# Optimization experiments

Measured on AMD Instinct MI355X. Metric: run time of the kernel, lower is better.

## Reference

```python
import jax, jax.numpy as jnp
import numpy as np

N_HEADS = 32
N_KV_HEADS = 8


def _rope_tables(T, half_dim):
    # standard rotary angle tables: theta_i = 10000^(-2i/D)
    inv_freq = 1.0 / (10000.0 ** (np.arange(half_dim, dtype=np.float32) / half_dim))
    ang = np.arange(T, dtype=np.float32)[:, None] * inv_freq[None, :]  # [T, D/2]
    return jnp.asarray(np.sin(ang)), jnp.asarray(np.cos(ang))


def setup_inputs() -> dict:
    key = jax.random.key(0)
    ks = jax.random.split(key, 5)
    B, T, C = 1, 2048, 2048
    hd = C // N_HEADS  # 64
    kv_dim = N_KV_HEADS * hd  # 512
    w_scale = 0.02
    x = jax.random.normal(ks[0], (B, T, C), dtype=jnp.float32)
    Wq = jax.random.normal(ks[1], (C, C), dtype=jnp.float32) * w_scale
    Wk = jax.random.normal(ks[2], (C, kv_dim), dtype=jnp.float32) * w_scale
    Wv = jax.random.normal(ks[3], (C, kv_dim), dtype=jnp.float32) * w_scale
    Wo = jax.random.normal(ks[4], (C, C), dtype=jnp.float32) * w_scale
    rope_sin, rope_cos = _rope_tables(T, hd // 2)
    return {"x": x, "Wq": Wq, "Wk": Wk, "Wv": Wv, "Wo": Wo,
            "rope_sin": rope_sin, "rope_cos": rope_cos, "swa_window": 1024}


def apply_rope(x, sin, cos):
    # x: [B, T, H, D]; sin/cos: [T, D/2]; interleaved-pair rotation
    B, T, H, D = x.shape
    xr = x.reshape(B, T, H, D // 2, 2)
    x1, x2 = xr[..., 0], xr[..., 1]
    s = sin[None, :, None, :]
    c = cos[None, :, None, :]
    o1 = x1 * c - x2 * s
    o2 = x1 * s + x2 * c
    return jnp.stack((o1, o2), axis=-1).reshape(B, T, H, D)


def reference(x, Wq, Wk, Wv, Wo, rope_sin, rope_cos, swa_window):
    B, T, C = x.shape
    hd = C // N_HEADS
    g = N_HEADS // N_KV_HEADS
    q = (x @ Wq).reshape(B, T, N_HEADS, hd)
    k = (x @ Wk).reshape(B, T, N_KV_HEADS, hd)
    v = (x @ Wv).reshape(B, T, N_KV_HEADS, hd)
    q = apply_rope(q, rope_sin, rope_cos)
    k = apply_rope(k, rope_sin, rope_cos)
    # GQA: expand kv heads (repeat_interleave along head dim)
    k = jnp.repeat(k, g, axis=2)
    v = jnp.repeat(v, g, axis=2)
    q = q.transpose(0, 2, 1, 3)  # [B, H, T, D]
    k = k.transpose(0, 2, 1, 3)
    v = v.transpose(0, 2, 1, 3)
    scores = jnp.einsum('bhqd,bhkd->bhqk', q, k) / jnp.sqrt(jnp.float32(hd))
    idx = jnp.arange(T)
    rel = idx[:, None] - idx[None, :]  # query_pos - key_pos
    # masked-out: future tokens (rel < 0) or older than the sliding window
    masked = (rel < 0) | (rel > swa_window)
    scores = jnp.where(masked[None, None], jnp.float32(-1e30), scores)
    attn = jax.nn.softmax(scores, axis=-1)
    out = jnp.einsum('bhqk,bhkd->bhqd', attn, v)
    out = out.transpose(0, 2, 1, 3).reshape(B, T, C)
    return out @ Wo
```

## Files before the change

kernel.cpp:

```cpp
#include <hip/hip_runtime.h>

typedef __attribute__((ext_vector_type(8))) short short8;
typedef __attribute__((ext_vector_type(4))) float f32x4;
typedef unsigned short u16;

#define T_SEQ 2048
#define C_DIM 2048
#define QKV_N 3072
#define HD 64


static __device__ __forceinline__ u16 f2bf(float f) {
    unsigned u = __builtin_bit_cast(unsigned, f);
    unsigned rounding = 0x7fffu + ((u >> 16) & 1u);
    return (u16)((u + rounding) >> 16);
}

static __device__ __forceinline__ void gld_lds16(void* lds, const void* g) {
    __builtin_amdgcn_global_load_lds(
        (const __attribute__((address_space(1))) unsigned int*)g,
        (__attribute__((address_space(3))) unsigned int*)lds, 16, 0, 0);
}


__global__ __launch_bounds__(256) void convert_bf16_k(const float* __restrict__ in,
                                                      u16* __restrict__ out) {
    int i = (blockIdx.x * 256 + threadIdx.x) * 4;
    f32x4 v = *(const f32x4*)(in + i);
    u16* o = out + i;
    o[0] = f2bf(v[0]); o[1] = f2bf(v[1]); o[2] = f2bf(v[2]); o[3] = f2bf(v[3]);
}


__global__ __launch_bounds__(256) void transpose_all(const float* __restrict__ Wq,
                                                     const float* __restrict__ Wk,
                                                     const float* __restrict__ Wv,
                                                     const float* __restrict__ Wo,
                                                     u16* __restrict__ Wt,
                                                     u16* __restrict__ Wot) {
    __shared__ float tile[32][33];
    int bx = blockIdx.x;
    const float* W; u16* D; int N, row_off;
    if (bx < 64)      { W = Wq; D = Wt;  N = 2048; row_off = 0;    }
    else if (bx < 80) { W = Wk; D = Wt;  N = 512;  row_off = 2048; bx -= 64; }
    else if (bx < 96) { W = Wv; D = Wt;  N = 512;  row_off = 2560; bx -= 80; }
    else              { W = Wo; D = Wot; N = 2048; row_off = 0;    bx -= 96; }
    int n0 = bx * 32, k0 = blockIdx.y * 32;
    int tx = threadIdx.x & 31, ty = threadIdx.x >> 5;
#pragma unroll
    for (int i = 0; i < 4; i++)
        tile[ty + i * 8][tx] = W[(size_t)(k0 + ty + i * 8) * N + n0 + tx];
    __syncthreads();
#pragma unroll
    for (int i = 0; i < 4; i++)
        D[(size_t)(row_off + n0 + ty + i * 8) * 2048 + k0 + tx] = f2bf(tile[tx][ty + i * 8]);
}


template <int NF>
__global__ __launch_bounds__(256) void gemm_bt(const u16* __restrict__ A,
                                               const u16* __restrict__ BT,
                                               float* __restrict__ C,
                                               int M, int N, int K) {
    __shared__ alignas(16) u16 As[2][128][64];
    __shared__ alignas(16) u16 Bs[2][32 * NF][64];
    const int m0 = blockIdx.x * 128;
    const int bn0 = blockIdx.y * (32 * NF);
    const int w = threadIdx.x >> 6, lane = threadIdx.x & 63;
    const int lo = lane & 15, hi = lane >> 4;
    const int wr = w >> 1, wc = w & 1;
    const int srcsw = ((lane & 7) ^ (lane >> 3)) * 8;

    f32x4 zero4 = {0.f, 0.f, 0.f, 0.f};
    f32x4 acc[4][NF];
#pragma unroll
    for (int m = 0; m < 4; m++)
#pragma unroll
        for (int n = 0; n < NF; n++) acc[m][n] = zero4;

    const int NSEG = 16 + 4 * NF;
    auto stage = [&](int buf, int k0) {
#pragma unroll
        for (int j = 0; j < NSEG / 4; j++) {
            int s = j * 4 + w;
            if (s < 16) {
                int row = s * 8 + (lane >> 3);
                gld_lds16((char*)&As[buf][0][0] + s * 1024,
                          A + (size_t)(m0 + row) * K + k0 + srcsw);
            } else {
                int s2 = s - 16;
                int row = s2 * 8 + (lane >> 3);
                gld_lds16((char*)&Bs[buf][0][0] + s2 * 1024,
                          BT + (size_t)(bn0 + row) * K + k0 + srcsw);
            }
        }
    };

    stage(0, 0);
    __syncthreads();
    const int nk = K >> 6;
    for (int t = 0; t < nk; t++) {
        const int cur = t & 1;
        if (t + 1 < nk) stage(cur ^ 1, (t + 1) * 64);
#pragma unroll
        for (int kk = 0; kk < 2; kk++) {
            const int csw = ((kk * 4 + hi) ^ (lo & 7)) << 4;
            short8 a[4], b[NF];
#pragma unroll
            for (int m = 0; m < 4; m++) {
                int r = wr * 64 + m * 16 + lo;
                a[m] = *(const short8*)((const char*)&As[cur][0][0] + r * 128 + csw);
            }
#pragma unroll
            for (int n = 0; n < NF; n++) {
                int r = wc * 16 * NF + n * 16 + lo;
                b[n] = *(const short8*)((const char*)&Bs[cur][0][0] + r * 128 + csw);
            }
#pragma unroll
            for (int m = 0; m < 4; m++)
#pragma unroll
                for (int n = 0; n < NF; n++)
                    acc[m][n] = __builtin_amdgcn_mfma_f32_16x16x32_bf16(a[m], b[n], acc[m][n], 0, 0, 0);
        }
        __syncthreads();
    }
#pragma unroll
    for (int m = 0; m < 4; m++)
#pragma unroll
        for (int n = 0; n < NF; n++) {
            int col = bn0 + wc * 16 * NF + n * 16 + lo;
#pragma unroll
            for (int r = 0; r < 4; r++) {
                int row = m0 + wr * 64 + m * 16 + hi * 4 + r;
                C[(size_t)row * N + col] = acc[m][n][r];
            }
        }
}


__global__ __launch_bounds__(256) void rope_conv(const float* __restrict__ qkv,
                                                 const float* __restrict__ sn,
                                                 const float* __restrict__ cs,
                                                 u16* __restrict__ qb,
                                                 u16* __restrict__ kb,
                                                 u16* __restrict__ vt) {
    int t = blockIdx.x / 6;
    int idx = (blockIdx.x % 6) * 256 + threadIdx.x;
    const float* row = qkv + (size_t)t * QKV_N;
    if (idx < 1024) {
        int h = idx >> 5, pr = idx & 31;
        float x1 = row[h * 64 + 2 * pr], x2 = row[h * 64 + 2 * pr + 1];
        float s = sn[t * 32 + pr], c = cs[t * 32 + pr];
        float o1 = (x1 * c - x2 * s) * 0.125f;
        float o2 = (x1 * s + x2 * c) * 0.125f;
        unsigned pack = (unsigned)f2bf(o1) | ((unsigned)f2bf(o2) << 16);
        *(unsigned*)(qb + (size_t)t * C_DIM + h * 64 + 2 * pr) = pack;
    } else if (idx < 1280) {
        int j = idx - 1024;
        int kh = j >> 5, pr = j & 31;
        float x1 = row[2048 + kh * 64 + 2 * pr], x2 = row[2048 + kh * 64 + 2 * pr + 1];
        float s = sn[t * 32 + pr], c = cs[t * 32 + pr];
        float o1 = x1 * c - x2 * s;
        float o2 = x1 * s + x2 * c;
        unsigned pack = (unsigned)f2bf(o1) | ((unsigned)f2bf(o2) << 16);
        *(unsigned*)(kb + ((size_t)kh * T_SEQ + t) * 64 + 2 * pr) = pack;
    } else {
        int j = idx - 1280;
        int kh = j >> 5, dl = (j & 31) * 2;
        float v0 = row[2560 + kh * 64 + dl], v1 = row[2560 + kh * 64 + dl + 1];
        vt[((size_t)kh * 64 + dl) * T_SEQ + t] = f2bf(v0);
        vt[((size_t)kh * 64 + dl + 1) * T_SEQ + t] = f2bf(v1);
    }
}


__global__ __launch_bounds__(256) void attn_fwd(const u16* __restrict__ qb,
                                                const u16* __restrict__ kb,
                                                const u16* __restrict__ vt,
                                                u16* __restrict__ ob,
                                                const int* __restrict__ winp) {
    __shared__ alignas(16) char KsB[2][8192];
    __shared__ alignas(16) char VsB[2][8192];
    __shared__ alignas(16) u16 Ps[4][16][64];
    const int window = *winp;
    const int h = blockIdx.y, kvh = h >> 2;
    const int q0 = blockIdx.x * 64;
    const int w = threadIdx.x >> 6, lane = threadIdx.x & 63;
    const int lo = lane & 15, hi = lane >> 4;

    const int qrow = q0 + w * 16 + lo;
    const short8 qa0 = *(const short8*)(qb + (size_t)qrow * C_DIM + h * HD + hi * 8);
    const short8 qa1 = *(const short8*)(qb + (size_t)qrow * C_DIM + h * HD + 32 + hi * 8);

    f32x4 zero4 = {0.f, 0.f, 0.f, 0.f};
    f32x4 acc[4];
#pragma unroll
    for (int dt = 0; dt < 4; dt++) acc[dt] = zero4;
    float lreg[4] = {0.f, 0.f, 0.f, 0.f};

    int kt0 = q0 - window; if (kt0 < 0) kt0 = 0; kt0 &= ~63;
    const int qlo_w = q0 + w * 16, qhi_w = qlo_w + 15;
    const int nt = (q0 + 64 - kt0) >> 6;

    auto stage = [&](int buf, int kt) {
#pragma unroll
        for (int j = 0; j < 2; j++) {
            int c = (w * 2 + j) * 64 + lane;
            int rr = c >> 3, sc = (c & 7) ^ (rr & 7);
            gld_lds16(KsB[buf] + (w * 2 + j) * 1024,
                      kb + ((size_t)kvh * T_SEQ + kt + rr) * 64 + sc * 8);
            gld_lds16(VsB[buf] + (w * 2 + j) * 1024,
                      vt + ((size_t)kvh * 64 + rr) * T_SEQ + kt + sc * 8);
        }
    };

    stage(0, kt0);
    __syncthreads();
    for (int i = 0; i < nt; i++) {
        const int kt = kt0 + i * 64;
        const int cur = i & 1;
        if (i + 1 < nt) stage(cur ^ 1, kt + 64);
        if (kt <= qhi_w && kt + 63 >= qlo_w - window) {
            const bool interior = (kt + 63 <= qlo_w) && (qhi_w - kt <= window);
            f32x4 s0, s1, s2, s3;
            __builtin_amdgcn_s_setprio(1);
            {
#define QK_TILE(SD, NT)                                                              \
                {                                                                    \
                    int key = (NT) * 16 + lo;                                        \
                    const short8 kf0 = *(const short8*)(KsB[cur] + key * 128 + ((hi ^ (key & 7)) << 4));       \
                    const short8 kf1 = *(const short8*)(KsB[cur] + key * 128 + (((4 + hi) ^ (key & 7)) << 4)); \
                    f32x4 z = zero4;                                                 \
                    z = __builtin_amdgcn_mfma_f32_16x16x32_bf16(qa0, kf0, z, 0, 0, 0);\
                    z = __builtin_amdgcn_mfma_f32_16x16x32_bf16(qa1, kf1, z, 0, 0, 0);\
                    SD = z;                                                          \
                }
                QK_TILE(s0, 0) QK_TILE(s1, 1) QK_TILE(s2, 2) QK_TILE(s3, 3)
#undef QK_TILE
            }
            __builtin_amdgcn_s_setprio(0);
            if (!interior) {
#define MASK_TILE(SD, NT)                                                            \
                {                                                                    \
                    int key = kt + (NT) * 16 + lo;                                   \
                    _Pragma("unroll")                                                \
                    for (int r = 0; r < 4; r++) {                                    \
                        int q = qlo_w + hi * 4 + r;                                  \
                        if ((unsigned)(q - key) > (unsigned)window) SD[r] = -1e30f;  \
                    }                                                                \
                }
                MASK_TILE(s0, 0) MASK_TILE(s1, 1) MASK_TILE(s2, 2) MASK_TILE(s3, 3)
#undef MASK_TILE
            }
#define EXP_TILE(SD, NT)                                                             \
            {                                                                        \
                _Pragma("unroll")                                                    \
                for (int r = 0; r < 4; r++) {                                        \
                    float p = __expf(SD[r]);                                         \
                    lreg[r] += p;                                                    \
                    int q16 = hi * 4 + r;                                            \
                    Ps[w][q16][((NT) * 16 + lo) ^ ((q16 & 7) << 3)] = f2bf(p);       \
                }                                                                    \
            }
            EXP_TILE(s0, 0) EXP_TILE(s1, 1) EXP_TILE(s2, 2) EXP_TILE(s3, 3)
#undef EXP_TILE
            const short8 pa0 = *(const short8*)&Ps[w][lo][(hi ^ (lo & 7)) << 3];
            const short8 pa1 = *(const short8*)&Ps[w][lo][((4 + hi) ^ (lo & 7)) << 3];
            __builtin_amdgcn_s_setprio(1);
#pragma unroll
            for (int dt = 0; dt < 4; dt++) {
                int d = dt * 16 + lo;
                const short8 vf0 = *(const short8*)(VsB[cur] + d * 128 + ((hi ^ (d & 7)) << 4));
                const short8 vf1 = *(const short8*)(VsB[cur] + d * 128 + (((4 + hi) ^ (d & 7)) << 4));
                acc[dt] = __builtin_amdgcn_mfma_f32_16x16x32_bf16(pa0, vf0, acc[dt], 0, 0, 0);
                acc[dt] = __builtin_amdgcn_mfma_f32_16x16x32_bf16(pa1, vf1, acc[dt], 0, 0, 0);
            }
            __builtin_amdgcn_s_setprio(0);
        }
        __syncthreads();
    }
    float inv[4];
#pragma unroll
    for (int r = 0; r < 4; r++) {
        float l = lreg[r];
        l += __shfl_xor(l, 1);
        l += __shfl_xor(l, 2);
        l += __shfl_xor(l, 4);
        l += __shfl_xor(l, 8);
        inv[r] = 1.0f / l;
    }
#pragma unroll
    for (int dt = 0; dt < 4; dt++)
#pragma unroll
        for (int r = 0; r < 4; r++) {
            int q = qlo_w + hi * 4 + r;
            ob[(size_t)q * C_DIM + h * HD + dt * 16 + lo] = f2bf(acc[dt][r] * inv[r]);
        }
}


extern "C" void kernel_launch(void* const* d_in, const int* in_sizes, int n_in,
                              void* d_out, int out_size, void* d_ws, size_t ws_size,
                              hipStream_t stream) {
    const float* x  = (const float*)d_in[0];
    const float* Wq = (const float*)d_in[1];
    const float* Wk = (const float*)d_in[2];
    const float* Wv = (const float*)d_in[3];
    const float* Wo = (const float*)d_in[4];
    const float* rs = (const float*)d_in[5];
    const float* rc = (const float*)d_in[6];
    const int*  win = (const int*)d_in[7];
    float* out = (float*)d_out;

    char* w = (char*)d_ws;
    u16*   xb   = (u16*)(w);
    u16*   Wt   = (u16*)(w + (8ull  << 20));
    u16*   Wot  = (u16*)(w + (20ull << 20));
    float* qkv  = (float*)(w + (28ull << 20));
    u16*   qb   = (u16*)(w + (52ull << 20));
    u16*   kbuf = (u16*)(w + (60ull << 20));
    u16*   vtb  = (u16*)(w + (62ull << 20));
    u16*   attb = (u16*)(w + (64ull << 20));

    convert_bf16_k<<<4096, 256, 0, stream>>>(x, xb);
    transpose_all<<<dim3(160, 64), 256, 0, stream>>>(Wq, Wk, Wv, Wo, Wt, Wot);
    gemm_bt<3><<<dim3(16, 32), 256, 0, stream>>>(xb, Wt, qkv, 2048, 3072, 2048);
    rope_conv<<<2048 * 6, 256, 0, stream>>>(qkv, rs, rc, qb, kbuf, vtb);
    attn_fwd<<<dim3(32, 32), 256, 0, stream>>>(qb, kbuf, vtb, attb, win);
    gemm_bt<2><<<dim3(16, 32), 256, 0, stream>>>(attb, Wot, out, 2048, 2048, 2048);
}
```

Before: 228.6 us.

## Persistent attention with atomic work queue, fuse prep kernels, tile V transpose

```diff
diff --git a/kernel.cpp b/kernel.cpp
--- a/kernel.cpp
+++ b/kernel.cpp
@@ -8,6 +8,7 @@
 #define C_DIM 2048
 #define QKV_N 3072
 #define HD 64
+#define N_UNITS 1024u
 
 
 static __device__ __forceinline__ u16 f2bf(float f) {
@@ -23,23 +24,24 @@
 }
 
 
-__global__ __launch_bounds__(256) void convert_bf16_k(const float* __restrict__ in,
-                                                      u16* __restrict__ out) {
-    int i = (blockIdx.x * 256 + threadIdx.x) * 4;
-    f32x4 v = *(const f32x4*)(in + i);
-    u16* o = out + i;
-    o[0] = f2bf(v[0]); o[1] = f2bf(v[1]); o[2] = f2bf(v[2]); o[3] = f2bf(v[3]);
-}
-
-
-__global__ __launch_bounds__(256) void transpose_all(const float* __restrict__ Wq,
-                                                     const float* __restrict__ Wk,
-                                                     const float* __restrict__ Wv,
-                                                     const float* __restrict__ Wo,
-                                                     u16* __restrict__ Wt,
-                                                     u16* __restrict__ Wot) {
+__global__ __launch_bounds__(256) void prep_all(const float* __restrict__ x,
+                                                const float* __restrict__ Wq,
+                                                const float* __restrict__ Wk,
+                                                const float* __restrict__ Wv,
+                                                const float* __restrict__ Wo,
+                                                u16* __restrict__ xb,
+                                                u16* __restrict__ Wt,
+                                                u16* __restrict__ Wot) {
     __shared__ float tile[32][33];
     int bx = blockIdx.x;
+    if (bx >= 160) {
+        int id = (bx - 160) * 64 + blockIdx.y;
+        int i = (id * 256 + threadIdx.x) * 4;
+        f32x4 v = *(const f32x4*)(x + i);
+        u16* o = xb + i;
+        o[0] = f2bf(v[0]); o[1] = f2bf(v[1]); o[2] = f2bf(v[2]); o[3] = f2bf(v[3]);
+        return;
+    }
     const float* W; u16* D; int N, row_off;
     if (bx < 64)      { W = Wq; D = Wt;  N = 2048; row_off = 0;    }
     else if (bx < 80) { W = Wk; D = Wt;  N = 512;  row_off = 2048; bx -= 64; }
@@ -138,16 +140,35 @@
 }
 
 
-__global__ __launch_bounds__(256) void rope_conv(const float* __restrict__ qkv,
-                                                 const float* __restrict__ sn,
-                                                 const float* __restrict__ cs,
-                                                 u16* __restrict__ qb,
-                                                 u16* __restrict__ kb,
-                                                 u16* __restrict__ vt) {
-    int t = blockIdx.x / 6;
-    int idx = (blockIdx.x % 6) * 256 + threadIdx.x;
+__global__ __launch_bounds__(256) void rope_all(const float* __restrict__ qkv,
+                                                const float* __restrict__ sn,
+                                                const float* __restrict__ cs,
+                                                u16* __restrict__ qb,
+                                                u16* __restrict__ kb,
+                                                u16* __restrict__ vt) {
+    __shared__ float tile[64][65];
+    const int by = blockIdx.y, bx = blockIdx.x;
+    if (by == 5) {
+        if (bx >= 256) return;
+        const int kvh = bx >> 5, t0 = (bx & 31) * 64;
+        const int tx = threadIdx.x & 63, ty = threadIdx.x >> 6;
+#pragma unroll
+        for (int i = 0; i < 16; i++) {
+            int r = ty * 16 + i;
+            tile[r][tx] = qkv[(size_t)(t0 + r) * QKV_N + 2560 + kvh * 64 + tx];
+        }
+        __syncthreads();
+#pragma unroll
+        for (int i = 0; i < 16; i++) {
+            int d = ty * 16 + i;
+            vt[((size_t)kvh * 64 + d) * T_SEQ + t0 + tx] = f2bf(tile[tx][d]);
+        }
+        return;
+    }
+    const int t = bx;
     const float* row = qkv + (size_t)t * QKV_N;
-    if (idx < 1024) {
+    if (by < 4) {
+        int idx = by * 256 + threadIdx.x;
         int h = idx >> 5, pr = idx & 31;
         float x1 = row[h * 64 + 2 * pr], x2 = row[h * 64 + 2 * pr + 1];
         float s = sn[t * 32 + pr], c = cs[t * 32 + pr];
@@ -155,21 +176,14 @@
         float o2 = (x1 * s + x2 * c) * 0.125f;
         unsigned pack = (unsigned)f2bf(o1) | ((unsigned)f2bf(o2) << 16);
         *(unsigned*)(qb + (size_t)t * C_DIM + h * 64 + 2 * pr) = pack;
-    } else if (idx < 1280) {
-        int j = idx - 1024;
-        int kh = j >> 5, pr = j & 31;
+    } else {
+        int kh = threadIdx.x >> 5, pr = threadIdx.x & 31;
         float x1 = row[2048 + kh * 64 + 2 * pr], x2 = row[2048 + kh * 64 + 2 * pr + 1];
         float s = sn[t * 32 + pr], c = cs[t * 32 + pr];
         float o1 = x1 * c - x2 * s;
         float o2 = x1 * s + x2 * c;
         unsigned pack = (unsigned)f2bf(o1) | ((unsigned)f2bf(o2) << 16);
         *(unsigned*)(kb + ((size_t)kh * T_SEQ + t) * 64 + 2 * pr) = pack;
-    } else {
-        int j = idx - 1280;
-        int kh = j >> 5, dl = (j & 31) * 2;
-        float v0 = row[2560 + kh * 64 + dl], v1 = row[2560 + kh * 64 + dl + 1];
-        vt[((size_t)kh * 64 + dl) * T_SEQ + t] = f2bf(v0);
-        vt[((size_t)kh * 64 + dl + 1) * T_SEQ + t] = f2bf(v1);
     }
 }
 
@@ -178,124 +192,134 @@
                                                 const u16* __restrict__ kb,
                                                 const u16* __restrict__ vt,
                                                 u16* __restrict__ ob,
-                                                const int* __restrict__ winp) {
+                                                const int* __restrict__ winp,
+                                                unsigned* __restrict__ counter) {
     __shared__ alignas(16) char KsB[2][8192];
     __shared__ alignas(16) char VsB[2][8192];
     __shared__ alignas(16) u16 Ps[4][16][64];
+    __shared__ unsigned s_u;
     const int window = *winp;
-    const int h = blockIdx.y, kvh = h >> 2;
-    const int q0 = blockIdx.x * 64;
     const int w = threadIdx.x >> 6, lane = threadIdx.x & 63;
     const int lo = lane & 15, hi = lane >> 4;
-
-    const int qrow = q0 + w * 16 + lo;
-    const short8 qa0 = *(const short8*)(qb + (size_t)qrow * C_DIM + h * HD + hi * 8);
-    const short8 qa1 = *(const short8*)(qb + (size_t)qrow * C_DIM + h * HD + 32 + hi * 8);
-
     f32x4 zero4 = {0.f, 0.f, 0.f, 0.f};
-    f32x4 acc[4];
-#pragma unroll
-    for (int dt = 0; dt < 4; dt++) acc[dt] = zero4;
-    float lreg[4] = {0.f, 0.f, 0.f, 0.f};
-
-    int kt0 = q0 - window; if (kt0 < 0) kt0 = 0; kt0 &= ~63;
-    const int qlo_w = q0 + w * 16, qhi_w = qlo_w + 15;
-    const int nt = (q0 + 64 - kt0) >> 6;
-
-    auto stage = [&](int buf, int kt) {
-#pragma unroll
-        for (int j = 0; j < 2; j++) {
-            int c = (w * 2 + j) * 64 + lane;
-            int rr = c >> 3, sc = (c & 7) ^ (rr & 7);
-            gld_lds16(KsB[buf] + (w * 2 + j) * 1024,
-                      kb + ((size_t)kvh * T_SEQ + kt + rr) * 64 + sc * 8);
-            gld_lds16(VsB[buf] + (w * 2 + j) * 1024,
-                      vt + ((size_t)kvh * 64 + rr) * T_SEQ + kt + sc * 8);
-        }
-    };
-
-    stage(0, kt0);
-    __syncthreads();
-    for (int i = 0; i < nt; i++) {
-        const int kt = kt0 + i * 64;
-        const int cur = i & 1;
-        if (i + 1 < nt) stage(cur ^ 1, kt + 64);
-        if (kt <= qhi_w && kt + 63 >= qlo_w - window) {
-            const bool interior = (kt + 63 <= qlo_w) && (qhi_w - kt <= window);
-            f32x4 s0, s1, s2, s3;
-            __builtin_amdgcn_s_setprio(1);
-            {
+
+    for (;;) {
+        if (threadIdx.x == 0) s_u = atomicAdd(counter, 1u);
+        __syncthreads();
+        const unsigned u = s_u;
+        if (u >= N_UNITS) break;
+        const int qi = 31 - (int)(u >> 5);
+        const int h = (int)(u & 31), kvh = h >> 2;
+        const int q0 = qi * 64;
+
+        const int qrow = q0 + w * 16 + lo;
+        const short8 qa0 = *(const short8*)(qb + (size_t)qrow * C_DIM + h * HD + hi * 8);
+        const short8 qa1 = *(const short8*)(qb + (size_t)qrow * C_DIM + h * HD + 32 + hi * 8);
+
+        f32x4 acc[4];
+#pragma unroll
+        for (int dt = 0; dt < 4; dt++) acc[dt] = zero4;
+        float lreg[4] = {0.f, 0.f, 0.f, 0.f};
+
+        int kt0 = q0 - window; if (kt0 < 0) kt0 = 0; kt0 &= ~63;
+        const int qlo_w = q0 + w * 16, qhi_w = qlo_w + 15;
+        const int nt = (q0 + 64 - kt0) >> 6;
+
+        auto stage = [&](int buf, int kt) {
+#pragma unroll
+            for (int j = 0; j < 2; j++) {
+                int c = (w * 2 + j) * 64 + lane;
+                int rr = c >> 3, sc = (c & 7) ^ (rr & 7);
+                gld_lds16(KsB[buf] + (w * 2 + j) * 1024,
+                          kb + ((size_t)kvh * T_SEQ + kt + rr) * 64 + sc * 8);
+                gld_lds16(VsB[buf] + (w * 2 + j) * 1024,
+                          vt + ((size_t)kvh * 64 + rr) * T_SEQ + kt + sc * 8);
+            }
+        };
+
+        stage(0, kt0);
+        __syncthreads();
+        for (int i = 0; i < nt; i++) {
+            const int kt = kt0 + i * 64;
+            const int cur = i & 1;
+            if (i + 1 < nt) stage(cur ^ 1, kt + 64);
+            if (kt <= qhi_w && kt + 63 >= qlo_w - window) {
+                const bool interior = (kt + 63 <= qlo_w) && (qhi_w - kt <= window);
+                f32x4 s0, s1, s2, s3;
+                __builtin_amdgcn_s_setprio(1);
+                {
 #define QK_TILE(SD, NT)                                                              \
+                    {                                                                \
+                        int key = (NT) * 16 + lo;                                    \
+                        const short8 kf0 = *(const short8*)(KsB[cur] + key * 128 + ((hi ^ (key & 7)) << 4));       \
+                        const short8 kf1 = *(const short8*)(KsB[cur] + key * 128 + (((4 + hi) ^ (key & 7)) << 4)); \
+                        f32x4 z = zero4;                                             \
+                        z = __builtin_amdgcn_mfma_f32_16x16x32_bf16(qa0, kf0, z, 0, 0, 0);\
+                        z = __builtin_amdgcn_mfma_f32_16x16x32_bf16(qa1, kf1, z, 0, 0, 0);\
+                        SD = z;                                                      \
+                    }
+                    QK_TILE(s0, 0) QK_TILE(s1, 1) QK_TILE(s2, 2) QK_TILE(s3, 3)
+#undef QK_TILE
+                }
+                __builtin_amdgcn_s_setprio(0);
+                if (!interior) {
+#define MASK_TILE(SD, NT)                                                            \
+                    {                                                                \
+                        int key = kt + (NT) * 16 + lo;                               \
+                        _Pragma("unroll")                                            \
+                        for (int r = 0; r < 4; r++) {                                \
+                            int q = qlo_w + hi * 4 + r;                              \
+                            if ((unsigned)(q - key) > (unsigned)window) SD[r] = -1e30f; \
+                        }                                                            \
+                    }
+                    MASK_TILE(s0, 0) MASK_TILE(s1, 1) MASK_TILE(s2, 2) MASK_TILE(s3, 3)
+#undef MASK_TILE
+                }
+#define EXP_TILE(SD, NT)                                                             \
                 {                                                                    \
-                    int key = (NT) * 16 + lo;                                        \
-                    const short8 kf0 = *(const short8*)(KsB[cur] + key * 128 + ((hi ^ (key & 7)) << 4));       \
-                    const short8 kf1 = *(const short8*)(KsB[cur] + key * 128 + (((4 + hi) ^ (key & 7)) << 4)); \
-                    f32x4 z = zero4;                                                 \
-                    z = __builtin_amdgcn_mfma_f32_16x16x32_bf16(qa0, kf0, z, 0, 0, 0);\
-                    z = __builtin_amdgcn_mfma_f32_16x16x32_bf16(qa1, kf1, z, 0, 0, 0);\
-                    SD = z;                                                          \
-                }
-                QK_TILE(s0, 0) QK_TILE(s1, 1) QK_TILE(s2, 2) QK_TILE(s3, 3)
-#undef QK_TILE
-            }
-            __builtin_amdgcn_s_setprio(0);
-            if (!interior) {
-#define MASK_TILE(SD, NT)                                                            \
-                {                                                                    \
-                    int key = kt + (NT) * 16 + lo;                                   \
                     _Pragma("unroll")                                                \
                     for (int r = 0; r < 4; r++) {                                    \
-                        int q = qlo_w + hi * 4 + r;                                  \
-                        if ((unsigned)(q - key) > (unsigned)window) SD[r] = -1e30f;  \
+                        float p = __expf(SD[r]);                                     \
+                        lreg[r] += p;                                                \
+                        int q16 = hi * 4 + r;                                        \
+                        Ps[w][q16][((NT) * 16 + lo) ^ ((q16 & 7) << 3)] = f2bf(p);   \
                     }                                                                \
                 }
-                MASK_TILE(s0, 0) MASK_TILE(s1, 1) MASK_TILE(s2, 2) MASK_TILE(s3, 3)
-#undef MASK_TILE
-            }
-#define EXP_TILE(SD, NT)                                                             \
-            {                                                                        \
-                _Pragma("unroll")                                                    \
-                for (int r = 0; r < 4; r++) {                                        \
-                    float p = __expf(SD[r]);                                         \
-                    lreg[r] += p;                                                    \
-                    int q16 = hi * 4 + r;                                            \
-                    Ps[w][q16][((NT) * 16 + lo) ^ ((q16 & 7) << 3)] = f2bf(p);       \
-                }                                                                    \
-            }
-            EXP_TILE(s0, 0) EXP_TILE(s1, 1) EXP_TILE(s2, 2) EXP_TILE(s3, 3)
+                EXP_TILE(s0, 0) EXP_TILE(s1, 1) EXP_TILE(s2, 2) EXP_TILE(s3, 3)
 #undef EXP_TILE
-            const short8 pa0 = *(const short8*)&Ps[w][lo][(hi ^ (lo & 7)) << 3];
-            const short8 pa1 = *(const short8*)&Ps[w][lo][((4 + hi) ^ (lo & 7)) << 3];
-            __builtin_amdgcn_s_setprio(1);
-#pragma unroll
-            for (int dt = 0; dt < 4; dt++) {
-                int d = dt * 16 + lo;
-                const short8 vf0 = *(const short8*)(VsB[cur] + d * 128 + ((hi ^ (d & 7)) << 4));
-                const short8 vf1 = *(const short8*)(VsB[cur] + d * 128 + (((4 + hi) ^ (d & 7)) << 4));
-                acc[dt] = __builtin_amdgcn_mfma_f32_16x16x32_bf16(pa0, vf0, acc[dt], 0, 0, 0);
-                acc[dt] = __builtin_amdgcn_mfma_f32_16x16x32_bf16(pa1, vf1, acc[dt], 0, 0, 0);
-            }
-            __builtin_amdgcn_s_setprio(0);
-        }
-        __syncthreads();
-    }
-    float inv[4];
-#pragma unroll
-    for (int r = 0; r < 4; r++) {
-        float l = lreg[r];
-        l += __shfl_xor(l, 1);
-        l += __shfl_xor(l, 2);
-        l += __shfl_xor(l, 4);
-        l += __shfl_xor(l, 8);
-        inv[r] = 1.0f / l;
-    }
-#pragma unroll
-    for (int dt = 0; dt < 4; dt++)
+                const short8 pa0 = *(const short8*)&Ps[w][lo][(hi ^ (lo & 7)) << 3];
+                const short8 pa1 = *(const short8*)&Ps[w][lo][((4 + hi) ^ (lo & 7)) << 3];
+                __builtin_amdgcn_s_setprio(1);
+#pragma unroll
+                for (int dt = 0; dt < 4; dt++) {
+                    int d = dt * 16 + lo;
+                    const short8 vf0 = *(const short8*)(VsB[cur] + d * 128 + ((hi ^ (d & 7)) << 4));
+                    const short8 vf1 = *(const short8*)(VsB[cur] + d * 128 + (((4 + hi) ^ (d & 7)) << 4));
+                    acc[dt] = __builtin_amdgcn_mfma_f32_16x16x32_bf16(pa0, vf0, acc[dt], 0, 0, 0);
+                    acc[dt] = __builtin_amdgcn_mfma_f32_16x16x32_bf16(pa1, vf1, acc[dt], 0, 0, 0);
+                }
+                __builtin_amdgcn_s_setprio(0);
+            }
+            __syncthreads();
+        }
+        float inv[4];
 #pragma unroll
         for (int r = 0; r < 4; r++) {
-            int q = qlo_w + hi * 4 + r;
-            ob[(size_t)q * C_DIM + h * HD + dt * 16 + lo] = f2bf(acc[dt][r] * inv[r]);
-        }
+            float l = lreg[r];
+            l += __shfl_xor(l, 1);
+            l += __shfl_xor(l, 2);
+            l += __shfl_xor(l, 4);
+            l += __shfl_xor(l, 8);
+            inv[r] = 1.0f / l;
+        }
+#pragma unroll
+        for (int dt = 0; dt < 4; dt++)
+#pragma unroll
+            for (int r = 0; r < 4; r++) {
+                int q = qlo_w + hi * 4 + r;
+                ob[(size_t)q * C_DIM + h * HD + dt * 16 + lo] = f2bf(acc[dt][r] * inv[r]);
+            }
+    }
 }
 
 
@@ -321,11 +345,12 @@
     u16*   kbuf = (u16*)(w + (60ull << 20));
     u16*   vtb  = (u16*)(w + (62ull << 20));
     u16*   attb = (u16*)(w + (64ull << 20));
-
-    convert_bf16_k<<<4096, 256, 0, stream>>>(x, xb);
-    transpose_all<<<dim3(160, 64), 256, 0, stream>>>(Wq, Wk, Wv, Wo, Wt, Wot);
+    unsigned* cnt = (unsigned*)(w + (28ull << 20));
+
+    prep_all<<<dim3(224, 64), 256, 0, stream>>>(x, Wq, Wk, Wv, Wo, xb, Wt, Wot);
     gemm_bt<3><<<dim3(16, 32), 256, 0, stream>>>(xb, Wt, qkv, 2048, 3072, 2048);
-    rope_conv<<<2048 * 6, 256, 0, stream>>>(qkv, rs, rc, qb, kbuf, vtb);
-    attn_fwd<<<dim3(32, 32), 256, 0, stream>>>(qb, kbuf, vtb, attb, win);
+    rope_all<<<dim3(2048, 6), 256, 0, stream>>>(qkv, rs, rc, qb, kbuf, vtb);
+    hipMemsetAsync(cnt, 0, 4, stream);
+    attn_fwd<<<768, 256, 0, stream>>>(qb, kbuf, vtb, attb, win, cnt);
     gemm_bt<2><<<dim3(16, 32), 256, 0, stream>>>(attb, Wot, out, 2048, 2048, 2048);
 }
```

Measured after the change: 227.1 us. No clear change (-0.7%).

## Fuse RoPE and bf16 conversion into QKV GEMM epilogue, merge prep kernels

Applied to the files above, without the earlier changes.

```diff
diff --git a/kernel.cpp b/kernel.cpp
--- a/kernel.cpp
+++ b/kernel.cpp
@@ -8,6 +8,7 @@
 #define C_DIM 2048
 #define QKV_N 3072
 #define HD 64
+#define QSCALE 0.18033688011112042f
 
 
 static __device__ __forceinline__ u16 f2bf(float f) {
@@ -23,23 +24,24 @@
 }
 
 
-__global__ __launch_bounds__(256) void convert_bf16_k(const float* __restrict__ in,
-                                                      u16* __restrict__ out) {
-    int i = (blockIdx.x * 256 + threadIdx.x) * 4;
-    f32x4 v = *(const f32x4*)(in + i);
-    u16* o = out + i;
-    o[0] = f2bf(v[0]); o[1] = f2bf(v[1]); o[2] = f2bf(v[2]); o[3] = f2bf(v[3]);
-}
-
-
-__global__ __launch_bounds__(256) void transpose_all(const float* __restrict__ Wq,
-                                                     const float* __restrict__ Wk,
-                                                     const float* __restrict__ Wv,
-                                                     const float* __restrict__ Wo,
-                                                     u16* __restrict__ Wt,
-                                                     u16* __restrict__ Wot) {
+__global__ __launch_bounds__(256) void prep_all(const float* __restrict__ x,
+                                                const float* __restrict__ Wq,
+                                                const float* __restrict__ Wk,
+                                                const float* __restrict__ Wv,
+                                                const float* __restrict__ Wo,
+                                                u16* __restrict__ xb,
+                                                u16* __restrict__ Wt,
+                                                u16* __restrict__ Wot) {
     __shared__ float tile[32][33];
     int bx = blockIdx.x;
+    if (bx >= 160) {
+        int id = (bx - 160) * 64 + blockIdx.y;
+        int i = (id * 256 + threadIdx.x) * 4;
+        f32x4 v = *(const f32x4*)(x + i);
+        u16* o = xb + i;
+        o[0] = f2bf(v[0]); o[1] = f2bf(v[1]); o[2] = f2bf(v[2]); o[3] = f2bf(v[3]);
+        return;
+    }
     const float* W; u16* D; int N, row_off;
     if (bx < 64)      { W = Wq; D = Wt;  N = 2048; row_off = 0;    }
     else if (bx < 80) { W = Wk; D = Wt;  N = 512;  row_off = 2048; bx -= 64; }
@@ -54,6 +56,104 @@
 #pragma unroll
     for (int i = 0; i < 4; i++)
         D[(size_t)(row_off + n0 + ty + i * 8) * 2048 + k0 + tx] = f2bf(tile[tx][ty + i * 8]);
+}
+
+
+__global__ __launch_bounds__(256) void gemm_qkv(const u16* __restrict__ A,
+                                                const u16* __restrict__ BT,
+                                                const float* __restrict__ sn,
+                                                const float* __restrict__ cs,
+                                                u16* __restrict__ qb,
+                                                u16* __restrict__ kb,
+                                                u16* __restrict__ vb) {
+    const int K = 2048;
+    __shared__ alignas(16) u16 As[2][128][64];
+    __shared__ alignas(16) u16 Bs[2][96][64];
+    const int m0 = blockIdx.x * 128;
+    const int bn0 = blockIdx.y * 96;
+    const int w = threadIdx.x >> 6, lane = threadIdx.x & 63;
+    const int lo = lane & 15, hi = lane >> 4;
+    const int wr = w >> 1, wc = w & 1;
+    const int srcsw = ((lane & 7) ^ (lane >> 3)) * 8;
+
+    f32x4 zero4 = {0.f, 0.f, 0.f, 0.f};
+    f32x4 acc[4][3];
+#pragma unroll
+    for (int m = 0; m < 4; m++)
+#pragma unroll
+        for (int n = 0; n < 3; n++) acc[m][n] = zero4;
+
+    auto stage = [&](int buf, int k0) {
+#pragma unroll
+        for (int j = 0; j < 7; j++) {
+            int s = j * 4 + w;
+            if (s < 16) {
+                int row = s * 8 + (lane >> 3);
+                gld_lds16((char*)&As[buf][0][0] + s * 1024,
+                          A + (size_t)(m0 + row) * K + k0 + srcsw);
+            } else {
+                int s2 = s - 16;
+                int row = s2 * 8 + (lane >> 3);
+                gld_lds16((char*)&Bs[buf][0][0] + s2 * 1024,
+                          BT + (size_t)(bn0 + row) * K + k0 + srcsw);
+            }
+        }
+    };
+
+    stage(0, 0);
+    __syncthreads();
+    const int nk = K >> 6;
+    for (int t = 0; t < nk; t++) {
+        const int cur = t & 1;
+        if (t + 1 < nk) stage(cur ^ 1, (t + 1) * 64);
+#pragma unroll
+        for (int kk = 0; kk < 2; kk++) {
+            const int csw = ((kk * 4 + hi) ^ (lo & 7)) << 4;
+            short8 a[4], b[3];
+#pragma unroll
+            for (int m = 0; m < 4; m++) {
+                int r = wr * 64 + m * 16 + lo;
+                a[m] = *(const short8*)((const char*)&As[cur][0][0] + r * 128 + csw);
+            }
+#pragma unroll
+            for (int n = 0; n < 3; n++) {
+                int r = wc * 48 + n * 16 + lo;
+                b[n] = *(const short8*)((const char*)&Bs[cur][0][0] + r * 128 + csw);
+            }
+#pragma unroll
+            for (int m = 0; m < 4; m++)
+#pragma unroll
+                for (int n = 0; n < 3; n++)
+                    acc[m][n] = __builtin_amdgcn_mfma_f32_16x16x32_bf16(a[m], b[n], acc[m][n], 0, 0, 0);
+        }
+        __syncthreads();
+    }
+    const bool odd = (lo & 1);
+#pragma unroll
+    for (int m = 0; m < 4; m++)
+#pragma unroll
+        for (int n = 0; n < 3; n++) {
+            const int col = bn0 + wc * 48 + n * 16 + lo;
+#pragma unroll
+            for (int r = 0; r < 4; r++) {
+                const int trow = m0 + wr * 64 + m * 16 + hi * 4 + r;
+                float v = acc[m][n][r];
+                float p = __shfl_xor(v, 1);
+                if (col >= 2560) {
+                    vb[(size_t)trow * 512 + (col - 2560)] = f2bf(v);
+                } else {
+                    const int pr = (col & 63) >> 1;
+                    const float s = sn[trow * 32 + pr], c = cs[trow * 32 + pr];
+                    float o = odd ? (p * s + v * c) : (v * c - p * s);
+                    if (col < 2048) {
+                        qb[(size_t)trow * C_DIM + col] = f2bf(o * QSCALE);
+                    } else {
+                        const int cc = col - 2048;
+                        kb[((size_t)(cc >> 6) * T_SEQ + trow) * 64 + (cc & 63)] = f2bf(o);
+                    }
+                }
+            }
+        }
 }
 
 
@@ -138,38 +238,21 @@
 }
 
 
-__global__ __launch_bounds__(256) void rope_conv(const float* __restrict__ qkv,
-                                                 const float* __restrict__ sn,
-                                                 const float* __restrict__ cs,
-                                                 u16* __restrict__ qb,
-                                                 u16* __restrict__ kb,
-                                                 u16* __restrict__ vt) {
-    int t = blockIdx.x / 6;
-    int idx = (blockIdx.x % 6) * 256 + threadIdx.x;
-    const float* row = qkv + (size_t)t * QKV_N;
-    if (idx < 1024) {
-        int h = idx >> 5, pr = idx & 31;
-        float x1 = row[h * 64 + 2 * pr], x2 = row[h * 64 + 2 * pr + 1];
-        float s = sn[t * 32 + pr], c = cs[t * 32 + pr];
-        float o1 = (x1 * c - x2 * s) * 0.125f;
-        float o2 = (x1 * s + x2 * c) * 0.125f;
-        unsigned pack = (unsigned)f2bf(o1) | ((unsigned)f2bf(o2) << 16);
-        *(unsigned*)(qb + (size_t)t * C_DIM + h * 64 + 2 * pr) = pack;
-    } else if (idx < 1280) {
-        int j = idx - 1024;
-        int kh = j >> 5, pr = j & 31;
-        float x1 = row[2048 + kh * 64 + 2 * pr], x2 = row[2048 + kh * 64 + 2 * pr + 1];
-        float s = sn[t * 32 + pr], c = cs[t * 32 + pr];
-        float o1 = x1 * c - x2 * s;
-        float o2 = x1 * s + x2 * c;
-        unsigned pack = (unsigned)f2bf(o1) | ((unsigned)f2bf(o2) << 16);
-        *(unsigned*)(kb + ((size_t)kh * T_SEQ + t) * 64 + 2 * pr) = pack;
-    } else {
-        int j = idx - 1280;
-        int kh = j >> 5, dl = (j & 31) * 2;
-        float v0 = row[2560 + kh * 64 + dl], v1 = row[2560 + kh * 64 + dl + 1];
-        vt[((size_t)kh * 64 + dl) * T_SEQ + t] = f2bf(v0);
-        vt[((size_t)kh * 64 + dl + 1) * T_SEQ + t] = f2bf(v1);
+__global__ __launch_bounds__(256) void vtrans(const u16* __restrict__ vb,
+                                              u16* __restrict__ vt) {
+    __shared__ unsigned tile[64][65];
+    const int kvh = blockIdx.x >> 5, t0 = (blockIdx.x & 31) * 64;
+    const int tx = threadIdx.x & 63, ty = threadIdx.x >> 6;
+#pragma unroll
+    for (int i = 0; i < 16; i++) {
+        int r = ty * 16 + i;
+        tile[r][tx] = vb[(size_t)(t0 + r) * 512 + kvh * 64 + tx];
+    }
+    __syncthreads();
+#pragma unroll
+    for (int i = 0; i < 16; i++) {
+        int d = ty * 16 + i;
+        vt[((size_t)kvh * 64 + d) * T_SEQ + t0 + tx] = (u16)tile[tx][d];
     }
 }
 
@@ -256,7 +339,7 @@
             {                                                                        \
                 _Pragma("unroll")                                                    \
                 for (int r = 0; r < 4; r++) {                                        \
-                    float p = __expf(SD[r]);                                         \
+                    float p = __builtin_amdgcn_exp2f(SD[r]);                         \
                     lreg[r] += p;                                                    \
                     int q16 = hi * 4 + r;                                            \
                     Ps[w][q16][((NT) * 16 + lo) ^ ((q16 & 7) << 3)] = f2bf(p);       \
@@ -316,16 +399,15 @@
     u16*   xb   = (u16*)(w);
     u16*   Wt   = (u16*)(w + (8ull  << 20));
     u16*   Wot  = (u16*)(w + (20ull << 20));
-    float* qkv  = (float*)(w + (28ull << 20));
-    u16*   qb   = (u16*)(w + (52ull << 20));
-    u16*   kbuf = (u16*)(w + (60ull << 20));
-    u16*   vtb  = (u16*)(w + (62ull << 20));
-    u16*   attb = (u16*)(w + (64ull << 20));
-
-    convert_bf16_k<<<4096, 256, 0, stream>>>(x, xb);
-    transpose_all<<<dim3(160, 64), 256, 0, stream>>>(Wq, Wk, Wv, Wo, Wt, Wot);
-    gemm_bt<3><<<dim3(16, 32), 256, 0, stream>>>(xb, Wt, qkv, 2048, 3072, 2048);
-    rope_conv<<<2048 * 6, 256, 0, stream>>>(qkv, rs, rc, qb, kbuf, vtb);
+    u16*   qb   = (u16*)(w + (28ull << 20));
+    u16*   kbuf = (u16*)(w + (36ull << 20));
+    u16*   vb   = (u16*)(w + (38ull << 20));
+    u16*   vtb  = (u16*)(w + (40ull << 20));
+    u16*   attb = (u16*)(w + (42ull << 20));
+
+    prep_all<<<dim3(224, 64), 256, 0, stream>>>(x, Wq, Wk, Wv, Wo, xb, Wt, Wot);
+    gemm_qkv<<<dim3(16, 32), 256, 0, stream>>>(xb, Wt, rs, rc, qb, kbuf, vb);
+    vtrans<<<256, 256, 0, stream>>>(vb, vtb);
     attn_fwd<<<dim3(32, 32), 256, 0, stream>>>(qb, kbuf, vtb, attb, win);
     gemm_bt<2><<<dim3(16, 32), 256, 0, stream>>>(attb, Wot, out, 2048, 2048, 2048);
 }
```

New measurement: 228.9 us. Within noise of the previous version (+0.1%).
